# Performance work log

Measured on AMD Instinct MI355X. Metric: run time of the kernel, lower is better.

The kernel has to match this reference:

```python
import jax, jax.numpy as jnp
import numpy as np

B, D, C = 4096, 2048, 64
L_HP, D_HP, OMEGA, EPSILON = 0.5, 1.0, 100.0, 0.1
LN_EPS = 1e-5
CLASS_COUNTS = [5000,4500,4050,3645,3280,2952,2657,2391,2152,1937,1743,1569,1412,1271,1144,1029,926,834,750,675,608,547,492,443,399,359,323,291,262,236,212,191,172,155,139,125,113,101,91,82,74,66,60,54,48,43,39,35,32,28,26,23,21,19,17,15,14,12,11,10,9,8,7,7]


def setup_inputs() -> dict:
    key = jax.random.key(0)
    k_x, k_y, k_b, k_u1, k_u2 = jax.random.split(key, 5)
    counts = jnp.asarray(CLASS_COUNTS, dtype=jnp.float32)
    # set_class_weights: tilde_C = 1/log(counts*d + eps), min-max normalized, scaled by l
    tilde = 1.0 / jnp.log(counts * D_HP + EPSILON)
    c = (tilde - jnp.min(tilde)) / (jnp.max(tilde) - jnp.min(tilde)) * L_HP
    # set_fs_classes: 1 where count <= omega
    fs_classes = jnp.where(counts <= OMEGA, 1, 0).astype(jnp.int32)
    x = jax.random.normal(k_x, (B, D), dtype=jnp.float32)
    y = jax.random.randint(k_y, (B,), 0, C)
    beta_idx = jax.random.randint(k_b, (B,), 0, B)
    u1 = jax.random.uniform(k_u1, (B,))
    u2 = jax.random.uniform(k_u2, (B,))
    alpha = jnp.where(u1 > 0.5, u2, jnp.ones((B,), jnp.float32))
    return {"x": x, "y": y, "alpha": alpha, "beta_idx": beta_idx, "c": c, "fs_classes": fs_classes}


def reference(x, y, alpha, beta_idx, c, fs_classes):
    n_batch, dim = x.shape
    num_classes = c.shape[0]
    # --- reconstruct ---
    mu = jnp.mean(x, axis=-1, keepdims=True)
    var = jnp.mean((x - mu) ** 2, axis=-1, keepdims=True)
    x_norm = (x - mu) / jnp.sqrt(var + LN_EPS) / jnp.sqrt(jnp.asarray(dim, x.dtype))
    sim = jnp.matmul(x_norm, x_norm.T)  # [B, B]
    # E[i, j] = eye[i, j] + fs_mask[j]  (broadcast over rows), thresholded to {0, 1}
    fs_mask = fs_classes[y].astype(x.dtype)  # [B]
    E = jnp.eye(n_batch, dtype=x.dtype) + fs_mask[None, :]
    E = jnp.where(E >= 1.0, 1.0, 0.0)
    sim = jax.nn.softmax(sim - 100000.0 * E, axis=-1)
    contrib = c[y]  # [B]
    reconstructions = jnp.matmul(sim, x)  # [B, D]
    R = reconstructions * contrib[:, None] + x * (1.0 - contrib)[:, None]
    # --- pairwise_mix: M @ R with M[i,:] = alpha[i]*e_i + (1-alpha[i])*e_{beta_idx[i]} ---
    y_oh = jax.nn.one_hot(y, num_classes, dtype=x.dtype)
    a = alpha[:, None]
    x_mix = a * R + (1.0 - a) * R[beta_idx]
    y_mix = a * y_oh + (1.0 - a) * y_oh[beta_idx]
    return (x_mix, y_mix)
```

## Files before the change

kernel.cpp:

```cpp
#include <hip/hip_runtime.h>
#include <cstdint>
#include <cstddef>

typedef float floatx4 __attribute__((ext_vector_type(4)));
typedef int intx8 __attribute__((ext_vector_type(8)));

#define NB 4096
#define ND 2048
#define NCLS 64
#define TSTRIDE 144

__device__ __forceinline__ void stage16(const void* g, void* l) {
  __builtin_amdgcn_global_load_lds(
      (__attribute__((address_space(1))) unsigned int*)g,
      (__attribute__((address_space(3))) unsigned int*)l, 16, 0, 0);
}

__device__ __forceinline__ unsigned char fp8x1(float f) {
  return (unsigned char)(__builtin_amdgcn_cvt_pk_fp8_f32(f, f, 0, false) & 0xFF);
}
__device__ __forceinline__ int fp8x4(float f0, float f1, float f2, float f3) {
  int d = __builtin_amdgcn_cvt_pk_fp8_f32(f0, f1, 0, false);
  return __builtin_amdgcn_cvt_pk_fp8_f32(f2, f3, d, true);
}

__device__ __forceinline__ void stage_step(const unsigned char* __restrict__ A,
                                           const unsigned char* __restrict__ B,
                                           int K, int m0, int n0, int k0,
                                           unsigned char* As,
                                           unsigned char* Bs) {
  const int t = threadIdx.x;
  const int w = t >> 6, lane = t & 63;
#pragma unroll
  for (int q = 0; q < 4; ++q) {
    const int slot = w * 256 + q * 64 + lane;
    const int row = slot >> 3;
    const int cc = (slot & 7) ^ (row & 7);
    stage16(A + (size_t)(m0 + row) * K + (k0 + cc * 16),
            As + (w * 256 + q * 64) * 16);
  }
#pragma unroll
  for (int q = 0; q < 4; ++q) {
    const int slot = w * 256 + q * 64 + lane;
    const int row = slot >> 3;
    const int cc = (slot & 7) ^ (row & 7);
    stage16(B + (size_t)(n0 + row) * K + (k0 + cc * 16),
            Bs + (w * 256 + q * 64) * 16);
  }
}

__device__ __forceinline__ void gemm_core8(const unsigned char* __restrict__ A,
                                           const unsigned char* __restrict__ B,
                                           int K, int m0, int n0,
                                           unsigned char* As0, unsigned char* Bs0,
                                           unsigned char* As1, unsigned char* Bs1,
                                           floatx4 acc[4][4]) {
  const int t = threadIdx.x;
  const int w = t >> 6;
  const int lane = t & 63;
  const int wm = w >> 1, wn = w & 1;
  const int lm = lane & 15, quad = lane >> 4;
  const int nk = K >> 7;

  stage_step(A, B, K, m0, n0, 0, As0, Bs0);

  for (int k = 0; k < nk; ++k) {
    __syncthreads();
    if (k + 1 < nk)
      stage_step(A, B, K, m0, n0, (k + 1) << 7, (k & 1) ? As0 : As1,
                 (k & 1) ? Bs0 : Bs1);
    unsigned char* Ac = (k & 1) ? As1 : As0;
    unsigned char* Bc = (k & 1) ? Bs1 : Bs0;

    intx8 af[4], bfr[4];
#pragma unroll
    for (int i = 0; i < 4; ++i) {
      const int row = wm * 64 + i * 16 + lm;
      const int c0 = (quad * 2) ^ (row & 7);
      const int4 lo = *(const int4*)(Ac + row * 128 + c0 * 16);
      const int4 hi = *(const int4*)(Ac + row * 128 + (c0 ^ 1) * 16);
      af[i][0] = lo.x; af[i][1] = lo.y; af[i][2] = lo.z; af[i][3] = lo.w;
      af[i][4] = hi.x; af[i][5] = hi.y; af[i][6] = hi.z; af[i][7] = hi.w;
    }
#pragma unroll
    for (int i = 0; i < 4; ++i) {
      const int row = wn * 64 + i * 16 + lm;
      const int c0 = (quad * 2) ^ (row & 7);
      const int4 lo = *(const int4*)(Bc + row * 128 + c0 * 16);
      const int4 hi = *(const int4*)(Bc + row * 128 + (c0 ^ 1) * 16);
      bfr[i][0] = lo.x; bfr[i][1] = lo.y; bfr[i][2] = lo.z; bfr[i][3] = lo.w;
      bfr[i][4] = hi.x; bfr[i][5] = hi.y; bfr[i][6] = hi.z; bfr[i][7] = hi.w;
    }
#pragma unroll
    for (int mi = 0; mi < 4; ++mi)
#pragma unroll
      for (int ni = 0; ni < 4; ++ni)
        acc[mi][ni] = __builtin_amdgcn_mfma_scale_f32_16x16x128_f8f6f4(
            af[mi], bfr[ni], acc[mi][ni], 0, 0, 0, 127, 0, 127);
  }
}


__global__ __launch_bounds__(256) void ln_kernel(
    const float* __restrict__ x, const int* __restrict__ y,
    const float* __restrict__ c, const int* __restrict__ fs,
    unsigned char* __restrict__ XN8, float* __restrict__ lrow,
    float* __restrict__ contrib, int* __restrict__ maskcol) {
  const int row = blockIdx.x, t = threadIdx.x;
  const float4* xr = (const float4*)(x + (size_t)row * ND);
  float4 v0 = xr[t], v1 = xr[t + 256];
  float s = v0.x + v0.y + v0.z + v0.w + v1.x + v1.y + v1.z + v1.w;
  float q = v0.x * v0.x + v0.y * v0.y + v0.z * v0.z + v0.w * v0.w +
            v1.x * v1.x + v1.y * v1.y + v1.z * v1.z + v1.w * v1.w;
#pragma unroll
  for (int o = 32; o > 0; o >>= 1) {
    s += __shfl_down(s, o);
    q += __shfl_down(q, o);
  }
  __shared__ float ss[4], qq[4];
  const int w = t >> 6;
  if ((t & 63) == 0) { ss[w] = s; qq[w] = q; }
  __syncthreads();
  s = ss[0] + ss[1] + ss[2] + ss[3];
  q = qq[0] + qq[1] + qq[2] + qq[3];
  const float mu = s * (1.0f / ND);
  const float var = q * (1.0f / ND) - mu * mu;
  const float sc =
      rsqrtf(var + 1e-5f) * 0.02209708691207961f * 32.0f;

  int* orow = (int*)(XN8 + (size_t)row * ND);
  orow[t] = fp8x4((v0.x - mu) * sc, (v0.y - mu) * sc, (v0.z - mu) * sc,
                  (v0.w - mu) * sc);
  orow[256 + t] = fp8x4((v1.x - mu) * sc, (v1.y - mu) * sc, (v1.z - mu) * sc,
                        (v1.w - mu) * sc);

  if (t == 0) {
    lrow[row] = 0.0f;
    const int yi = y[row];
    contrib[row] = c[yi];
    maskcol[row] = fs[yi];
  }
}

__global__ __launch_bounds__(256) void transpose_kernel(
    const float* __restrict__ x, unsigned char* __restrict__ XBT8) {
  __shared__ float tile[64][65];
  const int rb = blockIdx.x;
  const int cb = blockIdx.y;
  const int t = threadIdx.x;
  const int tx = t & 63, ty = t >> 6;
#pragma unroll
  for (int rr = ty; rr < 64; rr += 4)
    tile[rr][tx] = x[(size_t)(rb * 64 + rr) * ND + cb * 64 + tx];
  __syncthreads();
  const int ro = t >> 2;
  const int co = t & 3;
  int4 v;
  {
    const int j = co * 16;
    v.x = fp8x4(tile[j + 0][ro], tile[j + 1][ro], tile[j + 2][ro], tile[j + 3][ro]);
    v.y = fp8x4(tile[j + 4][ro], tile[j + 5][ro], tile[j + 6][ro], tile[j + 7][ro]);
    v.z = fp8x4(tile[j + 8][ro], tile[j + 9][ro], tile[j + 10][ro], tile[j + 11][ro]);
    v.w = fp8x4(tile[j + 12][ro], tile[j + 13][ro], tile[j + 14][ro], tile[j + 15][ro]);
  }
  *(int4*)(XBT8 + (size_t)(cb * 64 + ro) * NB + rb * 64 + co * 16) = v;
}

__global__ __launch_bounds__(256) void gemm_sim_kernel(
    const unsigned char* __restrict__ XN8, unsigned char* __restrict__ P8,
    float* __restrict__ lrow, const int* __restrict__ maskcol) {
  __shared__ unsigned char smem[65536];
  unsigned char* As0 = smem;
  unsigned char* Bs0 = smem + 16384;
  unsigned char* As1 = smem + 32768;
  unsigned char* Bs1 = smem + 49152;

  const int b = blockIdx.x;
  int bj = (int)((sqrtf(8.0f * (float)b + 1.0f) - 1.0f) * 0.5f);
  while ((bj + 1) * (bj + 2) / 2 <= b) ++bj;
  while (bj * (bj + 1) / 2 > b) --bj;
  const int bi = b - bj * (bj + 1) / 2;
  const int m0 = bi * 128, n0 = bj * 128;

  floatx4 acc[4][4];
#pragma unroll
  for (int i = 0; i < 4; ++i)
#pragma unroll
    for (int j = 0; j < 4; ++j) acc[i][j] = 0.0f;

  gemm_core8(XN8, XN8, ND, m0, n0, As0, Bs0, As1, Bs1, acc);

  const int t = threadIdx.x, w = t >> 6, lane = t & 63;
  const int wm = w >> 1, wn = w & 1, lm = lane & 15, quad = lane >> 4;

  int cmj[4];
#pragma unroll
  for (int ni = 0; ni < 4; ++ni) cmj[ni] = maskcol[n0 + wn * 64 + ni * 16 + lm];
  int rmk[4][4];
#pragma unroll
  for (int mi = 0; mi < 4; ++mi)
#pragma unroll
    for (int r = 0; r < 4; ++r)
      rmk[mi][r] = maskcol[m0 + wm * 64 + mi * 16 + quad * 4 + r];

  float rs[4][4];
#pragma unroll
  for (int mi = 0; mi < 4; ++mi)
#pragma unroll
    for (int r = 0; r < 4; ++r) rs[mi][r] = 0.0f;

#pragma unroll
  for (int ni = 0; ni < 4; ++ni) {
    const int gcol = n0 + wn * 64 + ni * 16 + lm;
#pragma unroll
    for (int mi = 0; mi < 4; ++mi) {
#pragma unroll
      for (int r = 0; r < 4; ++r) {
        const int grow = m0 + wm * 64 + mi * 16 + quad * 4 + r;
        float e = (grow == gcol) ? 0.0f
                                 : __expf(acc[mi][ni][r] * 0.0009765625f);
        acc[mi][ni][r] = e;
        rs[mi][r] += cmj[ni] ? 0.0f : e;
      }
    }
  }
#pragma unroll
  for (int mi = 0; mi < 4; ++mi)
#pragma unroll
    for (int r = 0; r < 4; ++r) {
      float vsum = rs[mi][r];
      vsum += __shfl_xor(vsum, 1);
      vsum += __shfl_xor(vsum, 2);
      vsum += __shfl_xor(vsum, 4);
      vsum += __shfl_xor(vsum, 8);
      if (lm == 0)
        atomicAdd(&lrow[m0 + wm * 64 + mi * 16 + quad * 4 + r], vsum);
    }

  __syncthreads();
#pragma unroll
  for (int ni = 0; ni < 4; ++ni) {
    const int col = wn * 64 + ni * 16 + lm;
#pragma unroll
    for (int mi = 0; mi < 4; ++mi)
#pragma unroll
      for (int r = 0; r < 4; ++r) {
        const int row = wm * 64 + mi * 16 + quad * 4 + r;
        smem[row * TSTRIDE + col] = fp8x1(cmj[ni] ? 0.0f : acc[mi][ni][r]);
      }
  }
  __syncthreads();
#pragma unroll
  for (int it = 0; it < 4; ++it) {
    const int row = it * 32 + (t >> 3), ch = t & 7;
    int4 v = *(const int4*)(smem + row * TSTRIDE + ch * 16);
    *(int4*)(P8 + (size_t)(m0 + row) * NB + n0 + ch * 16) = v;
  }

  if (bi != bj) {
    __syncthreads();
#pragma unroll
    for (int ni = 0; ni < 4; ++ni) {
      const int tc = wn * 64 + ni * 16 + lm;
      float cs = 0.0f;
#pragma unroll
      for (int mi = 0; mi < 4; ++mi) {
        float g0 = rmk[mi][0] ? 0.0f : acc[mi][ni][0];
        float g1 = rmk[mi][1] ? 0.0f : acc[mi][ni][1];
        float g2 = rmk[mi][2] ? 0.0f : acc[mi][ni][2];
        float g3 = rmk[mi][3] ? 0.0f : acc[mi][ni][3];
        cs += g0 + g1 + g2 + g3;
        *(int*)(smem + tc * TSTRIDE + wm * 64 + mi * 16 + quad * 4) =
            fp8x4(g0, g1, g2, g3);
      }
      cs += __shfl_xor(cs, 16);
      cs += __shfl_xor(cs, 32);
      if (quad == 0) atomicAdd(&lrow[n0 + tc], cs);
    }
    __syncthreads();
#pragma unroll
    for (int it = 0; it < 4; ++it) {
      const int row = it * 32 + (t >> 3), ch = t & 7;
      int4 v = *(const int4*)(smem + row * TSTRIDE + ch * 16);
      *(int4*)(P8 + (size_t)(n0 + row) * NB + m0 + ch * 16) = v;
    }
  }
}

__global__ __launch_bounds__(256) void gemm_recon_kernel(
    const unsigned char* __restrict__ P8, const unsigned char* __restrict__ XBT8,
    const float* __restrict__ x, const float* __restrict__ lrow,
    const float* __restrict__ contrib, float* __restrict__ R) {
  __shared__ unsigned char smem[65536];
  unsigned char* As0 = smem;
  unsigned char* Bs0 = smem + 16384;
  unsigned char* As1 = smem + 32768;
  unsigned char* Bs1 = smem + 49152;
  const int m0 = blockIdx.y * 128, n0 = blockIdx.x * 128;
  floatx4 acc[4][4];
#pragma unroll
  for (int i = 0; i < 4; ++i)
#pragma unroll
    for (int j = 0; j < 4; ++j) acc[i][j] = 0.0f;

  gemm_core8(P8, XBT8, NB, m0, n0, As0, Bs0, As1, Bs1, acc);

  const int t = threadIdx.x, w = t >> 6, lane = t & 63;
  const int wm = w >> 1, wn = w & 1, lm = lane & 15, quad = lane >> 4;
#pragma unroll
  for (int mi = 0; mi < 4; ++mi) {
#pragma unroll
    for (int r = 0; r < 4; ++r) {
      const int grow = m0 + wm * 64 + mi * 16 + quad * 4 + r;
      const float inv = 1.0f / lrow[grow];
      const float ci = contrib[grow];
#pragma unroll
      for (int ni = 0; ni < 4; ++ni) {
        const int gcol = n0 + wn * 64 + ni * 16 + lm;
        const float rec = acc[mi][ni][r] * inv;
        const float xv = x[(size_t)grow * ND + gcol];
        R[(size_t)grow * ND + gcol] = rec * ci + xv * (1.0f - ci);
      }
    }
  }
}

__global__ __launch_bounds__(256) void mix_kernel(
    const float* __restrict__ R, const float* __restrict__ alpha,
    const int* __restrict__ beta_idx, const int* __restrict__ y,
    float* __restrict__ out) {
  const int i = blockIdx.x, t = threadIdx.x;
  const float a = alpha[i];
  const int bi = beta_idx[i];
  const float4* Ri = (const float4*)(R + (size_t)i * ND);
  const float4* Rb = (const float4*)(R + (size_t)bi * ND);
  float4* o = (float4*)(out + (size_t)i * ND);
  const float b = 1.0f - a;
#pragma unroll
  for (int j = 0; j < 2; ++j) {
    const int idx = t + j * 256;
    float4 r = Ri[idx], g = Rb[idx], ov;
    ov.x = a * r.x + b * g.x;
    ov.y = a * r.y + b * g.y;
    ov.z = a * r.z + b * g.z;
    ov.w = a * r.w + b * g.w;
    o[idx] = ov;
  }
  if (t < NCLS) {
    const int yi = y[i], yb = y[bi];
    const float v = a * (t == yi ? 1.0f : 0.0f) + b * (t == yb ? 1.0f : 0.0f);
    out[(size_t)NB * ND + (size_t)i * NCLS + t] = v;
  }
}

extern "C" void kernel_launch(void* const* d_in, const int* in_sizes, int n_in,
                              void* d_out, int out_size, void* d_ws,
                              size_t ws_size, hipStream_t stream) {
  const float* x = (const float*)d_in[0];
  const int* y = (const int*)d_in[1];
  const float* alpha = (const float*)d_in[2];
  const int* beta = (const int*)d_in[3];
  const float* c = (const float*)d_in[4];
  const int* fs = (const int*)d_in[5];
  float* out = (float*)d_out;
  char* ws = (char*)d_ws;

  unsigned char* XN8  = (unsigned char*)(ws + 0);
  unsigned char* XBT8 = (unsigned char*)(ws + 8388608);
  unsigned char* P8   = (unsigned char*)(ws + 16777216);
  float* R  = (float*)(ws + 33554432);
  float* LR = (float*)(ws + 67108864);
  float* CT = (float*)(ws + 67108864 + 16384);
  int* MC   = (int*)(ws + 67108864 + 32768);

  ln_kernel<<<NB, 256, 0, stream>>>(x, y, c, fs, XN8, LR, CT, MC);
  transpose_kernel<<<dim3(64, 32), 256, 0, stream>>>(x, XBT8);
  gemm_sim_kernel<<<528, 256, 0, stream>>>(XN8, P8, LR, MC);
  gemm_recon_kernel<<<dim3(16, 32), 256, 0, stream>>>(P8, XBT8, x, LR, CT, R);
  mix_kernel<<<NB, 256, 0, stream>>>(R, alpha, beta, y, out);
}
```

Before: 191.0 us.

## Store R in bf16 via LDS staging, fuse prep kernels, remap recon blocks per XCD

Merges the layernorm and transpose kernels into one launch. The reconstruction GEMM now writes R as bf16 through an LDS staging buffer so stores are coalesced and 16 bytes wide. Its blocks are remapped so neighbouring column tiles land on the same XCD for better L2 reuse. The mix kernel reads the bf16 R, which halves R traffic but adds a bf16 rounding step on the output path.

Measured after the change: 179.1 us. -6.3%, faster.

```diff
diff --git a/kernel.cpp b/kernel.cpp
--- a/kernel.cpp
+++ b/kernel.cpp
@@ -2,6 +2,8 @@
 #include <cstdint>
 #include <cstddef>
 
+typedef __bf16 bf16;
+typedef __bf16 bf16x8 __attribute__((ext_vector_type(8)));
 typedef float floatx4 __attribute__((ext_vector_type(4)));
 typedef int intx8 __attribute__((ext_vector_type(8)));
 
@@ -9,6 +11,7 @@
 #define ND 2048
 #define NCLS 64
 #define TSTRIDE 144
+#define OS 136
 
 __device__ __forceinline__ void stage16(const void* g, void* l) {
   __builtin_amdgcn_global_load_lds(
@@ -101,69 +104,70 @@
 }
 
 
-__global__ __launch_bounds__(256) void ln_kernel(
+__global__ __launch_bounds__(256) void prep_kernel(
     const float* __restrict__ x, const int* __restrict__ y,
     const float* __restrict__ c, const int* __restrict__ fs,
-    unsigned char* __restrict__ XN8, float* __restrict__ lrow,
-    float* __restrict__ contrib, int* __restrict__ maskcol) {
-  const int row = blockIdx.x, t = threadIdx.x;
-  const float4* xr = (const float4*)(x + (size_t)row * ND);
-  float4 v0 = xr[t], v1 = xr[t + 256];
-  float s = v0.x + v0.y + v0.z + v0.w + v1.x + v1.y + v1.z + v1.w;
-  float q = v0.x * v0.x + v0.y * v0.y + v0.z * v0.z + v0.w * v0.w +
-            v1.x * v1.x + v1.y * v1.y + v1.z * v1.z + v1.w * v1.w;
-#pragma unroll
-  for (int o = 32; o > 0; o >>= 1) {
-    s += __shfl_down(s, o);
-    q += __shfl_down(q, o);
-  }
-  __shared__ float ss[4], qq[4];
-  const int w = t >> 6;
-  if ((t & 63) == 0) { ss[w] = s; qq[w] = q; }
-  __syncthreads();
-  s = ss[0] + ss[1] + ss[2] + ss[3];
-  q = qq[0] + qq[1] + qq[2] + qq[3];
-  const float mu = s * (1.0f / ND);
-  const float var = q * (1.0f / ND) - mu * mu;
-  const float sc =
-      rsqrtf(var + 1e-5f) * 0.02209708691207961f * 32.0f;
-
-  int* orow = (int*)(XN8 + (size_t)row * ND);
-  orow[t] = fp8x4((v0.x - mu) * sc, (v0.y - mu) * sc, (v0.z - mu) * sc,
-                  (v0.w - mu) * sc);
-  orow[256 + t] = fp8x4((v1.x - mu) * sc, (v1.y - mu) * sc, (v1.z - mu) * sc,
-                        (v1.w - mu) * sc);
-
-  if (t == 0) {
-    lrow[row] = 0.0f;
-    const int yi = y[row];
-    contrib[row] = c[yi];
-    maskcol[row] = fs[yi];
-  }
-}
-
-__global__ __launch_bounds__(256) void transpose_kernel(
-    const float* __restrict__ x, unsigned char* __restrict__ XBT8) {
+    unsigned char* __restrict__ XN8, unsigned char* __restrict__ XBT8,
+    float* __restrict__ lrow, float* __restrict__ contrib,
+    int* __restrict__ maskcol) {
   __shared__ float tile[64][65];
-  const int rb = blockIdx.x;
-  const int cb = blockIdx.y;
   const int t = threadIdx.x;
-  const int tx = t & 63, ty = t >> 6;
-#pragma unroll
-  for (int rr = ty; rr < 64; rr += 4)
-    tile[rr][tx] = x[(size_t)(rb * 64 + rr) * ND + cb * 64 + tx];
-  __syncthreads();
-  const int ro = t >> 2;
-  const int co = t & 3;
-  int4 v;
-  {
-    const int j = co * 16;
-    v.x = fp8x4(tile[j + 0][ro], tile[j + 1][ro], tile[j + 2][ro], tile[j + 3][ro]);
-    v.y = fp8x4(tile[j + 4][ro], tile[j + 5][ro], tile[j + 6][ro], tile[j + 7][ro]);
-    v.z = fp8x4(tile[j + 8][ro], tile[j + 9][ro], tile[j + 10][ro], tile[j + 11][ro]);
-    v.w = fp8x4(tile[j + 12][ro], tile[j + 13][ro], tile[j + 14][ro], tile[j + 15][ro]);
-  }
-  *(int4*)(XBT8 + (size_t)(cb * 64 + ro) * NB + rb * 64 + co * 16) = v;
+
+  if (blockIdx.x < NB) {
+    const int row = blockIdx.x;
+    const float4* xr = (const float4*)(x + (size_t)row * ND);
+    float4 v0 = xr[t], v1 = xr[t + 256];
+    float s = v0.x + v0.y + v0.z + v0.w + v1.x + v1.y + v1.z + v1.w;
+    float q = v0.x * v0.x + v0.y * v0.y + v0.z * v0.z + v0.w * v0.w +
+              v1.x * v1.x + v1.y * v1.y + v1.z * v1.z + v1.w * v1.w;
+#pragma unroll
+    for (int o = 32; o > 0; o >>= 1) {
+      s += __shfl_down(s, o);
+      q += __shfl_down(q, o);
+    }
+    const int w = t >> 6;
+    if ((t & 63) == 0) { tile[0][w] = s; tile[1][w] = q; }
+    __syncthreads();
+    s = tile[0][0] + tile[0][1] + tile[0][2] + tile[0][3];
+    q = tile[1][0] + tile[1][1] + tile[1][2] + tile[1][3];
+    const float mu = s * (1.0f / ND);
+    const float var = q * (1.0f / ND) - mu * mu;
+    const float sc =
+        rsqrtf(var + 1e-5f) * 0.02209708691207961f * 32.0f;
+
+    int* orow = (int*)(XN8 + (size_t)row * ND);
+    orow[t] = fp8x4((v0.x - mu) * sc, (v0.y - mu) * sc, (v0.z - mu) * sc,
+                    (v0.w - mu) * sc);
+    orow[256 + t] = fp8x4((v1.x - mu) * sc, (v1.y - mu) * sc, (v1.z - mu) * sc,
+                          (v1.w - mu) * sc);
+
+    if (t == 0) {
+      lrow[row] = 0.0f;
+      const int yi = y[row];
+      contrib[row] = c[yi];
+      maskcol[row] = fs[yi];
+    }
+  } else {
+    const int b2 = blockIdx.x - NB;
+    const int rb = b2 & 63;
+    const int cb = b2 >> 6;
+    const int tx = t & 63, ty = t >> 6;
+#pragma unroll
+    for (int rr = ty; rr < 64; rr += 4)
+      tile[rr][tx] = x[(size_t)(rb * 64 + rr) * ND + cb * 64 + tx];
+    __syncthreads();
+    const int ro = t >> 2;
+    const int co = t & 3;
+    int4 v;
+    {
+      const int j = co * 16;
+      v.x = fp8x4(tile[j + 0][ro], tile[j + 1][ro], tile[j + 2][ro], tile[j + 3][ro]);
+      v.y = fp8x4(tile[j + 4][ro], tile[j + 5][ro], tile[j + 6][ro], tile[j + 7][ro]);
+      v.z = fp8x4(tile[j + 8][ro], tile[j + 9][ro], tile[j + 10][ro], tile[j + 11][ro]);
+      v.w = fp8x4(tile[j + 12][ro], tile[j + 13][ro], tile[j + 14][ro], tile[j + 15][ro]);
+    }
+    *(int4*)(XBT8 + (size_t)(cb * 64 + ro) * NB + rb * 64 + co * 16) = v;
+  }
 }
 
 __global__ __launch_bounds__(256) void gemm_sim_kernel(
@@ -290,13 +294,20 @@
 __global__ __launch_bounds__(256) void gemm_recon_kernel(
     const unsigned char* __restrict__ P8, const unsigned char* __restrict__ XBT8,
     const float* __restrict__ x, const float* __restrict__ lrow,
-    const float* __restrict__ contrib, float* __restrict__ R) {
+    const float* __restrict__ contrib, bf16* __restrict__ R) {
   __shared__ unsigned char smem[65536];
   unsigned char* As0 = smem;
   unsigned char* Bs0 = smem + 16384;
   unsigned char* As1 = smem + 32768;
   unsigned char* Bs1 = smem + 49152;
-  const int m0 = blockIdx.y * 128, n0 = blockIdx.x * 128;
+
+  const int id = blockIdx.x;
+  const int xcd = id & 7;
+  const int s = id >> 3;
+  const int bx = xcd * 2 + (s & 1);
+  const int by = s >> 1;
+  const int m0 = by * 128, n0 = bx * 128;
+
   floatx4 acc[4][4];
 #pragma unroll
   for (int i = 0; i < 4; ++i)
@@ -307,45 +318,58 @@
 
   const int t = threadIdx.x, w = t >> 6, lane = t & 63;
   const int wm = w >> 1, wn = w & 1, lm = lane & 15, quad = lane >> 4;
+
+  __syncthreads();
+  bf16* osm = (bf16*)smem;
 #pragma unroll
   for (int mi = 0; mi < 4; ++mi) {
 #pragma unroll
     for (int r = 0; r < 4; ++r) {
-      const int grow = m0 + wm * 64 + mi * 16 + quad * 4 + r;
+      const int lrow_i = wm * 64 + mi * 16 + quad * 4 + r;
+      const int grow = m0 + lrow_i;
       const float inv = 1.0f / lrow[grow];
       const float ci = contrib[grow];
 #pragma unroll
       for (int ni = 0; ni < 4; ++ni) {
-        const int gcol = n0 + wn * 64 + ni * 16 + lm;
+        const int lcol = wn * 64 + ni * 16 + lm;
         const float rec = acc[mi][ni][r] * inv;
-        const float xv = x[(size_t)grow * ND + gcol];
-        R[(size_t)grow * ND + gcol] = rec * ci + xv * (1.0f - ci);
+        const float xv = x[(size_t)grow * ND + n0 + lcol];
+        osm[lrow_i * OS + lcol] = (bf16)(rec * ci + xv * (1.0f - ci));
       }
     }
   }
+  __syncthreads();
+#pragma unroll
+  for (int it = 0; it < 8; ++it) {
+    const int row = it * 16 + (t >> 4), ch = t & 15;
+    int4 v = *(const int4*)(osm + row * OS + ch * 8);
+    *(int4*)(R + (size_t)(m0 + row) * ND + n0 + ch * 8) = v;
+  }
 }
 
 __global__ __launch_bounds__(256) void mix_kernel(
-    const float* __restrict__ R, const float* __restrict__ alpha,
+    const bf16* __restrict__ R, const float* __restrict__ alpha,
     const int* __restrict__ beta_idx, const int* __restrict__ y,
     float* __restrict__ out) {
   const int i = blockIdx.x, t = threadIdx.x;
   const float a = alpha[i];
   const int bi = beta_idx[i];
-  const float4* Ri = (const float4*)(R + (size_t)i * ND);
-  const float4* Rb = (const float4*)(R + (size_t)bi * ND);
-  float4* o = (float4*)(out + (size_t)i * ND);
+  const bf16x8* Ri = (const bf16x8*)(R + (size_t)i * ND);
+  const bf16x8* Rb = (const bf16x8*)(R + (size_t)bi * ND);
   const float b = 1.0f - a;
-#pragma unroll
-  for (int j = 0; j < 2; ++j) {
-    const int idx = t + j * 256;
-    float4 r = Ri[idx], g = Rb[idx], ov;
-    ov.x = a * r.x + b * g.x;
-    ov.y = a * r.y + b * g.y;
-    ov.z = a * r.z + b * g.z;
-    ov.w = a * r.w + b * g.w;
-    o[idx] = ov;
-  }
+  bf16x8 r = Ri[t], g = Rb[t];
+  float4 o0, o1;
+  o0.x = a * (float)r[0] + b * (float)g[0];
+  o0.y = a * (float)r[1] + b * (float)g[1];
+  o0.z = a * (float)r[2] + b * (float)g[2];
+  o0.w = a * (float)r[3] + b * (float)g[3];
+  o1.x = a * (float)r[4] + b * (float)g[4];
+  o1.y = a * (float)r[5] + b * (float)g[5];
+  o1.z = a * (float)r[6] + b * (float)g[6];
+  o1.w = a * (float)r[7] + b * (float)g[7];
+  float4* o = (float4*)(out + (size_t)i * ND + t * 8);
+  o[0] = o0;
+  o[1] = o1;
   if (t < NCLS) {
     const int yi = y[i], yb = y[bi];
     const float v = a * (t == yi ? 1.0f : 0.0f) + b * (t == yb ? 1.0f : 0.0f);
@@ -368,14 +392,13 @@
   unsigned char* XN8  = (unsigned char*)(ws + 0);
   unsigned char* XBT8 = (unsigned char*)(ws + 8388608);
   unsigned char* P8   = (unsigned char*)(ws + 16777216);
-  float* R  = (float*)(ws + 33554432);
-  float* LR = (float*)(ws + 67108864);
-  float* CT = (float*)(ws + 67108864 + 16384);
-  int* MC   = (int*)(ws + 67108864 + 32768);
-
-  ln_kernel<<<NB, 256, 0, stream>>>(x, y, c, fs, XN8, LR, CT, MC);
-  transpose_kernel<<<dim3(64, 32), 256, 0, stream>>>(x, XBT8);
+  bf16* R   = (bf16*)(ws + 33554432);
+  float* LR = (float*)(ws + 50331648);
+  float* CT = (float*)(ws + 50331648 + 16384);
+  int* MC   = (int*)(ws + 50331648 + 32768);
+
+  prep_kernel<<<NB + 2048, 256, 0, stream>>>(x, y, c, fs, XN8, XBT8, LR, CT, MC);
   gemm_sim_kernel<<<528, 256, 0, stream>>>(XN8, P8, LR, MC);
-  gemm_recon_kernel<<<dim3(16, 32), 256, 0, stream>>>(P8, XBT8, x, LR, CT, R);
+  gemm_recon_kernel<<<512, 256, 0, stream>>>(P8, XBT8, x, LR, CT, R);
   mix_kernel<<<NB, 256, 0, stream>>>(R, alpha, beta, y, out);
 }
```
